# Performance work log

Hardware: AMD Instinct MI355X
Metric: run time of the kernel (lower is better)

The kernel has to match this reference:

```python
import jax, jax.numpy as jnp
import numpy as np

B, H, Wd, C = 32, 32, 32, 128
N = H * Wd  # flattened spatial dim = Dense units per channel


def setup_inputs() -> dict:
    key = jax.random.key(0)
    k1, k2 = jax.random.split(key)
    inputs = jax.random.normal(k1, (B, H, Wd, C), dtype=jnp.float32)
    # Per-channel Dense weights stacked: [C, N, N], glorot-ish scale
    W = jax.random.normal(k2, (C, N, N), dtype=jnp.float32) * (1.0 / np.sqrt(N))
    b = jnp.zeros((C, N), dtype=jnp.float32)
    return {"inputs": inputs, "W": W, "b": b}


def reference(inputs, W, b):
    Bb, h, w, c = inputs.shape
    n = h * w
    x = inputs.reshape(Bb, n, c)                      # [B, N, C]
    # one batched GEMM over channels instead of C separate Dense calls
    y = jnp.einsum('bnc,cnm->bcm', x, W) + b          # [B, C, N]
    y = jax.nn.relu(y)
    y = y.reshape(Bb, c, h, w).transpose(0, 2, 3, 1)  # [B, H, W, C]
    # original concatenates each new channel at the FRONT -> reversed channel order
    return y[..., ::-1]
```

## Files before the change

### kernel.cpp

```cpp
#include <hip/hip_runtime.h>

#define Bb 32
#define NN 1024
#define CC 128
#define KS 64
#define MT 128
#define NSTEP (NN / KS)

typedef __bf16 bf16x8 __attribute__((ext_vector_type(8)));
typedef __bf16 bf16x4 __attribute__((ext_vector_type(4)));
typedef float f32x16 __attribute__((ext_vector_type(16)));
typedef float f32x4 __attribute__((ext_vector_type(4)));
typedef unsigned short u16x8 __attribute__((ext_vector_type(8)));

__global__ __launch_bounds__(256) void transpose_x(const float* __restrict__ in,
                                                   __bf16* __restrict__ xbf) {
    __shared__ float tile[64 * 132];
    const int b  = blockIdx.x >> 4;
    const int n0 = (blockIdx.x & 15) << 6;
    const int t  = threadIdx.x;

#pragma unroll
    for (int p = 0; p < 8; ++p) {
        int f     = p * 256 + t;
        int n_off = f >> 5;
        int c4    = (f & 31) << 2;
        f32x4 v = *reinterpret_cast<const f32x4*>(in + ((size_t)(b * NN + n0 + n_off) * CC + c4));
        *reinterpret_cast<f32x4*>(&tile[n_off * 132 + c4]) = v;
    }
    __syncthreads();

    const int c = t >> 1, half = t & 1;
    const size_t obase = ((size_t)c * Bb + b) * NN + n0;
#pragma unroll
    for (int q = 0; q < 4; ++q) {
        int nb = half * 32 + q * 8;
        bf16x8 o;
#pragma unroll
        for (int j = 0; j < 8; ++j) o[j] = (__bf16)tile[(nb + j) * 132 + c];
        *reinterpret_cast<bf16x8*>(xbf + obase + nb) = o;
    }
}

__global__ __launch_bounds__(256) void cwdense_part(const float* __restrict__ W,
                                                    const float* __restrict__ bias,
                                                    const __bf16* __restrict__ xbf,
                                                    float* __restrict__ part) {
    __shared__ __bf16 wlds[MT * 64];

    const int x     = blockIdx.x;
    const int xcd   = x & 7;
    const int i     = x >> 3;
    const int c     = xcd * 16 + (i & 15);
    const int mtile = i >> 4;
    const int m0    = mtile * MT;

    const int t    = threadIdx.x;
    const int w    = t >> 6;
    const int lane = t & 63;
    const int lm   = lane & 31;
    const int lh   = lane >> 5;
    const int m_loc = w * 32 + lm;

    const float* wpanel = W + (size_t)c * NN * NN + m0;
    const __bf16* xrow  = xbf + (size_t)(c * Bb + lm) * NN;

    const int mq  = t & 31;
    const int kq2 = t >> 5;

    f32x16 acc;
#pragma unroll
    for (int r = 0; r < 16; ++r) acc[r] = 0.0f;

    for (int step = 0; step < NSTEP; ++step) {
        const int k0 = step * KS;

        f32x4 q[2][4];
#pragma unroll
        for (int qi = 0; qi < 2; ++qi)
#pragma unroll
            for (int r = 0; r < 4; ++r)
                q[qi][r] = __builtin_nontemporal_load(reinterpret_cast<const f32x4*>(
                    wpanel + (size_t)(k0 + (kq2 * 2 + qi) * 4 + r) * NN + mq * 4));

        __syncthreads();

#pragma unroll
        for (int qi = 0; qi < 2; ++qi) {
            const int kkbase = (kq2 * 2 + qi) * 4;
#pragma unroll
            for (int j = 0; j < 4; ++j) {
                const int m = mq * 4 + j;
                bf16x4 o;
#pragma unroll
                for (int r = 0; r < 4; ++r) o[r] = (__bf16)q[qi][r][j];
                const int slot = (kkbase >> 3) ^ (m & 7) ^ ((m >> 3) & 7);
                *reinterpret_cast<bf16x4*>(&wlds[m * 64 + slot * 8 + (kkbase & 7)]) = o;
            }
        }
        __syncthreads();

#pragma unroll
        for (int mi = 0; mi < 4; ++mi) {
            const int kk = mi * 16 + lh * 8;
            bf16x8 a = *reinterpret_cast<const bf16x8*>(xrow + k0 + kk);
            const int slot = (kk >> 3) ^ (m_loc & 7) ^ ((m_loc >> 3) & 7);
            bf16x8 bfrag = *reinterpret_cast<const bf16x8*>(&wlds[m_loc * 64 + slot * 8]);
            acc = __builtin_amdgcn_mfma_f32_32x32x16_bf16(a, bfrag, acc, 0, 0, 0);
        }
    }

    const int m  = m0 + m_loc;
    const float bv = bias[(size_t)c * NN + m];
    float* pc = part + (size_t)c * Bb * NN;
#pragma unroll
    for (int r = 0; r < 16; ++r) {
        const int brow = (r & 3) + 8 * (r >> 2) + 4 * lh;
        float v = acc[r] + bv;
        v = v > 0.0f ? v : 0.0f;
        pc[(size_t)brow * NN + m] = v;
    }
}

__global__ __launch_bounds__(256) void permute_out(const float* __restrict__ part,
                                                   float* __restrict__ out) {
    __shared__ float st[CC * 65];
    const int b  = blockIdx.x >> 4;
    const int m0 = (blockIdx.x & 15) * 64;
    const int t  = threadIdx.x;

    {
        const int mm = t & 63, cr = t >> 6;
#pragma unroll 4
        for (int j = 0; j < 32; ++j) {
            const int c = cr * 32 + j;
            st[c * 65 + mm] = part[((size_t)c * Bb + b) * NN + m0 + mm];
        }
    }
    __syncthreads();
    {
        const int co4 = (t & 31) * 4, mr = t >> 5;
#pragma unroll
        for (int jj = 0; jj < 8; ++jj) {
            const int mloc = mr + 8 * jj;
            f32x4 v;
#pragma unroll
            for (int i = 0; i < 4; ++i)
                v[i] = st[(CC - 1 - co4 - i) * 65 + mloc];
            __builtin_nontemporal_store(v, reinterpret_cast<f32x4*>(
                out + ((size_t)b * NN + m0 + mloc) * CC + co4));
        }
    }
}

template <int USE_XBF>
__global__ __launch_bounds__(256) void cwdense_direct(const float* __restrict__ W,
                                                      const float* __restrict__ bias,
                                                      const float* __restrict__ xin,
                                                      const __bf16* __restrict__ xbf,
                                                      float* __restrict__ out) {
    __shared__ __bf16 wlds[MT * 64];
    const int x = blockIdx.x, xcd = x & 7, i = x >> 3;
    const int c = xcd * 16 + (i & 15), mtile = i >> 4, m0 = mtile * MT;
    const int t = threadIdx.x, w = t >> 6, lane = t & 63;
    const int lm = lane & 31, lh = lane >> 5, m_loc = w * 32 + lm;
    const float* wpanel = W + (size_t)c * NN * NN + m0;
    const int mq = t & 31, kq2 = t >> 5;

    f32x16 acc;
#pragma unroll
    for (int r = 0; r < 16; ++r) acc[r] = 0.0f;

    for (int step = 0; step < NSTEP; ++step) {
        const int k0 = step * KS;
        f32x4 q[2][4];
#pragma unroll
        for (int qi = 0; qi < 2; ++qi)
#pragma unroll
            for (int r = 0; r < 4; ++r)
                q[qi][r] = *reinterpret_cast<const f32x4*>(
                    wpanel + (size_t)(k0 + (kq2 * 2 + qi) * 4 + r) * NN + mq * 4);
        __syncthreads();
#pragma unroll
        for (int qi = 0; qi < 2; ++qi) {
            const int kkbase = (kq2 * 2 + qi) * 4;
#pragma unroll
            for (int j = 0; j < 4; ++j) {
                const int m = mq * 4 + j;
                bf16x4 o;
#pragma unroll
                for (int r = 0; r < 4; ++r) o[r] = (__bf16)q[qi][r][j];
                const int slot = (kkbase >> 3) ^ (m & 7) ^ ((m >> 3) & 7);
                *reinterpret_cast<bf16x4*>(&wlds[m * 64 + slot * 8 + (kkbase & 7)]) = o;
            }
        }
        __syncthreads();
#pragma unroll
        for (int mi = 0; mi < 4; ++mi) {
            const int kk = mi * 16 + lh * 8;
            bf16x8 a;
            if (USE_XBF) {
                a = *reinterpret_cast<const bf16x8*>(xbf + ((size_t)(c * Bb + lm) * NN + k0 + kk));
            } else {
                u16x8 tmp;
#pragma unroll
                for (int e = 0; e < 8; ++e) {
                    float f = xin[((size_t)lm * NN + (k0 + kk + e)) * CC + c];
                    unsigned u = __builtin_bit_cast(unsigned, f);
                    u = (u + 0x7FFFu + ((u >> 16) & 1u)) >> 16;
                    tmp[e] = (unsigned short)u;
                }
                a = __builtin_bit_cast(bf16x8, tmp);
            }
            const int slot = (kk >> 3) ^ (m_loc & 7) ^ ((m_loc >> 3) & 7);
            bf16x8 bfrag = *reinterpret_cast<const bf16x8*>(&wlds[m_loc * 64 + slot * 8]);
            acc = __builtin_amdgcn_mfma_f32_32x32x16_bf16(a, bfrag, acc, 0, 0, 0);
        }
    }
    const int m = m0 + m_loc;
    const float bv = bias[(size_t)c * NN + m];
    const int co = (CC - 1) - c;
#pragma unroll
    for (int r = 0; r < 16; ++r) {
        const int brow = (r & 3) + 8 * (r >> 2) + 4 * lh;
        float v = acc[r] + bv;
        v = v > 0.0f ? v : 0.0f;
        out[(size_t)brow * (NN * CC) + (size_t)m * CC + co] = v;
    }
}

extern "C" void kernel_launch(void* const* d_in, const int* in_sizes, int n_in,
                              void* d_out, int out_size, void* d_ws, size_t ws_size,
                              hipStream_t stream) {
    const float* xinp = (const float*)d_in[0];
    const float* W    = (const float*)d_in[1];
    const float* bias = (const float*)d_in[2];
    float* out        = (float*)d_out;

    const size_t part_bytes = (size_t)CC * Bb * NN * sizeof(float);
    const size_t xbf_bytes  = (size_t)CC * Bb * NN * sizeof(__bf16);

    if (ws_size >= part_bytes + xbf_bytes) {
        float*  part = (float*)d_ws;
        __bf16* xbf  = (__bf16*)((char*)d_ws + part_bytes);
        transpose_x<<<512, 256, 0, stream>>>(xinp, xbf);
        cwdense_part<<<1024, 256, 0, stream>>>(W, bias, xbf, part);
        permute_out<<<512, 256, 0, stream>>>(part, out);
    } else if (ws_size >= xbf_bytes) {
        __bf16* xbf = (__bf16*)d_ws;
        transpose_x<<<512, 256, 0, stream>>>(xinp, xbf);
        cwdense_direct<1><<<1024, 256, 0, stream>>>(W, bias, xinp, xbf, out);
    } else {
        cwdense_direct<0><<<1024, 256, 0, stream>>>(W, bias, xinp, nullptr, out);
    }
}
```

Measured before the change: 109.4 us.

## Double-buffer W panel loads in registers and store intermediate output as bf16

The GEMM main loop now keeps two register sets for W tiles, so the global load for the next K step is issued before the MFMAs of the current step, overlapping HBM latency with compute. The intermediate per-channel result buffer is stored in bf16 instead of fp32, halving the workspace write and the reread in the permute kernel, which now uses vectorized 16-byte loads. Keeping a second register tile raises register pressure, and rounding the output to bf16 adds precision loss before the final fp32 write.

```diff
diff --git a/kernel.cpp b/kernel.cpp
--- a/kernel.cpp
+++ b/kernel.cpp
@@ -45,7 +45,7 @@
 __global__ __launch_bounds__(256) void cwdense_part(const float* __restrict__ W,
                                                     const float* __restrict__ bias,
                                                     const __bf16* __restrict__ xbf,
-                                                    float* __restrict__ part) {
+                                                    __bf16* __restrict__ part) {
     __shared__ __bf16 wlds[MT * 64];
 
     const int x     = blockIdx.x;
@@ -72,19 +72,18 @@
 #pragma unroll
     for (int r = 0; r < 16; ++r) acc[r] = 0.0f;
 
-    for (int step = 0; step < NSTEP; ++step) {
-        const int k0 = step * KS;
-
-        f32x4 q[2][4];
-#pragma unroll
-        for (int qi = 0; qi < 2; ++qi)
-#pragma unroll
-            for (int r = 0; r < 4; ++r)
-                q[qi][r] = __builtin_nontemporal_load(reinterpret_cast<const f32x4*>(
-                    wpanel + (size_t)(k0 + (kq2 * 2 + qi) * 4 + r) * NN + mq * 4));
-
-        __syncthreads();
-
+    f32x4 qA[8], qB[8];
+
+    auto load_tile = [&](f32x4 (&q)[8], int k0) {
+#pragma unroll
+        for (int r = 0; r < 8; ++r) {
+            const int kk = (kq2 * 2 + (r >> 2)) * 4 + (r & 3);
+            q[r] = __builtin_nontemporal_load(reinterpret_cast<const f32x4*>(
+                wpanel + (size_t)(k0 + kk) * NN + mq * 4));
+        }
+    };
+
+    auto store_tile = [&](const f32x4 (&q)[8]) {
 #pragma unroll
         for (int qi = 0; qi < 2; ++qi) {
             const int kkbase = (kq2 * 2 + qi) * 4;
@@ -93,13 +92,14 @@
                 const int m = mq * 4 + j;
                 bf16x4 o;
 #pragma unroll
-                for (int r = 0; r < 4; ++r) o[r] = (__bf16)q[qi][r][j];
+                for (int r = 0; r < 4; ++r) o[r] = (__bf16)q[qi * 4 + r][j];
                 const int slot = (kkbase >> 3) ^ (m & 7) ^ ((m >> 3) & 7);
                 *reinterpret_cast<bf16x4*>(&wlds[m * 64 + slot * 8 + (kkbase & 7)]) = o;
             }
         }
-        __syncthreads();
-
+    };
+
+    auto mfma_step = [&](int k0) {
 #pragma unroll
         for (int mi = 0; mi < 4; ++mi) {
             const int kk = mi * 16 + lh * 8;
@@ -108,21 +108,38 @@
             bf16x8 bfrag = *reinterpret_cast<const bf16x8*>(&wlds[m_loc * 64 + slot * 8]);
             acc = __builtin_amdgcn_mfma_f32_32x32x16_bf16(a, bfrag, acc, 0, 0, 0);
         }
+    };
+
+    load_tile(qA, 0);
+
+#pragma unroll 1
+    for (int s = 0; s < NSTEP; s += 2) {
+        __syncthreads();
+        store_tile(qA);
+        __syncthreads();
+        load_tile(qB, (s + 1) * KS);
+        mfma_step(s * KS);
+
+        __syncthreads();
+        store_tile(qB);
+        __syncthreads();
+        if (s + 2 < NSTEP) load_tile(qA, (s + 2) * KS);
+        mfma_step((s + 1) * KS);
     }
 
     const int m  = m0 + m_loc;
     const float bv = bias[(size_t)c * NN + m];
-    float* pc = part + (size_t)c * Bb * NN;
+    __bf16* pc = part + (size_t)c * Bb * NN;
 #pragma unroll
     for (int r = 0; r < 16; ++r) {
         const int brow = (r & 3) + 8 * (r >> 2) + 4 * lh;
         float v = acc[r] + bv;
         v = v > 0.0f ? v : 0.0f;
-        pc[(size_t)brow * NN + m] = v;
-    }
-}
-
-__global__ __launch_bounds__(256) void permute_out(const float* __restrict__ part,
+        pc[(size_t)brow * NN + m] = (__bf16)v;
+    }
+}
+
+__global__ __launch_bounds__(256) void permute_out(const __bf16* __restrict__ part,
                                                    float* __restrict__ out) {
     __shared__ float st[CC * 65];
     const int b  = blockIdx.x >> 4;
@@ -130,11 +147,14 @@
     const int t  = threadIdx.x;
 
     {
-        const int mm = t & 63, cr = t >> 6;
-#pragma unroll 4
-        for (int j = 0; j < 32; ++j) {
-            const int c = cr * 32 + j;
-            st[c * 65 + mm] = part[((size_t)c * Bb + b) * NN + m0 + mm];
+        const int c = t >> 1, half = t & 1;
+        const __bf16* src = part + ((size_t)c * Bb + b) * NN + m0 + half * 32;
+#pragma unroll
+        for (int q = 0; q < 4; ++q) {
+            bf16x8 v = *reinterpret_cast<const bf16x8*>(src + q * 8);
+#pragma unroll
+            for (int j = 0; j < 8; ++j)
+                st[c * 65 + half * 32 + q * 8 + j] = (float)v[j];
         }
     }
     __syncthreads();
@@ -237,11 +257,11 @@
     const float* bias = (const float*)d_in[2];
     float* out        = (float*)d_out;
 
-    const size_t part_bytes = (size_t)CC * Bb * NN * sizeof(float);
+    const size_t part_bytes = (size_t)CC * Bb * NN * sizeof(__bf16);
     const size_t xbf_bytes  = (size_t)CC * Bb * NN * sizeof(__bf16);
 
     if (ws_size >= part_bytes + xbf_bytes) {
-        float*  part = (float*)d_ws;
+        __bf16* part = (__bf16*)d_ws;
         __bf16* xbf  = (__bf16*)((char*)d_ws + part_bytes);
         transpose_x<<<512, 256, 0, stream>>>(xinp, xbf);
         cwdense_part<<<1024, 256, 0, stream>>>(W, bias, xbf, part);
```

New measurement: 110.8 us. Within noise of the previous version (+1.3%).
